# Performance work log

Measured on AMD Instinct MI355X. Metric: run time of the kernel, lower is better.

## Reference

```python
import jax, jax.numpy as jnp
import numpy as np

T_MIN, T_MAX = 0.6, 1.6
SIM_LO, SIM_HI = 0.5, 0.9
LN_EPS = 1e-5


def _layernorm(x, gamma, beta):
    mu = jnp.mean(x, axis=-1, keepdims=True)
    var = jnp.mean((x - mu) ** 2, axis=-1, keepdims=True)
    return (x - mu) * jax.lax.rsqrt(var + LN_EPS) * gamma + beta


def _cos_sim(a, b, eps=1e-8):
    num = jnp.sum(a * b, axis=-1)
    na = jnp.maximum(jnp.sqrt(jnp.sum(a * a, axis=-1)), eps)
    nb = jnp.maximum(jnp.sqrt(jnp.sum(b * b, axis=-1)), eps)
    return num / (na * nb)


def setup_inputs() -> dict:
    key = jax.random.key(0)
    B, L, D = 2, 4096, 512
    ks = jax.random.split(key, 10)
    s = 0.02
    return {
        "x": jax.random.normal(ks[0], (B, L, D), dtype=jnp.float32),
        "Wq": jax.random.normal(ks[1], (D, D), dtype=jnp.float32) * s,
        "Wk": jax.random.normal(ks[2], (D, D), dtype=jnp.float32) * s,
        "Wv": jax.random.normal(ks[3], (D, D), dtype=jnp.float32) * s,
        "Wp": jax.random.normal(ks[4], (D, D), dtype=jnp.float32) * s,
        "W1": jax.random.normal(ks[5], (4 * D, D), dtype=jnp.float32) * s,
        "b1": jnp.zeros((4 * D,), dtype=jnp.float32),
        "W2": jax.random.normal(ks[6], (D, 4 * D), dtype=jnp.float32) * s,
        "b2": jnp.zeros((D,), dtype=jnp.float32),
        "gamma": jnp.ones((D,), dtype=jnp.float32),
        "beta": jnp.zeros((D,), dtype=jnp.float32),
    }


def reference(x, Wq, Wk, Wv, Wp, W1, b1, W2, b2, gamma, beta):
    B, L, D = x.shape
    xn = _layernorm(x, gamma, beta)
    # TinyAttn with T=1.0, causal=True (torch Linear: x @ W.T)
    Q = jnp.einsum("bld,ed->ble", xn, Wq)
    K = jnp.einsum("bld,ed->ble", xn, Wk)
    V = jnp.einsum("bld,ed->ble", xn, Wv)
    scores = jnp.einsum("bld,bmd->blm", Q, K) / jnp.sqrt(jnp.asarray(D, x.dtype))
    causal = jnp.triu(jnp.ones((L, L), dtype=bool), 1)
    scores = jnp.where(causal, jnp.asarray(-1e30, x.dtype), scores)
    attn = jax.nn.softmax(scores, axis=-1)  # [B, L, L]
    out = jnp.einsum("blm,bmd->bld", attn, V)
    out = jnp.einsum("bld,ed->ble", out, Wp)
    ctx = x + out
    h = _layernorm(ctx, gamma, beta)
    h = jax.nn.gelu(jnp.einsum("bld,fd->blf", h, W1) + b1, approximate=False)
    ctx = ctx + jnp.einsum("blf,df->bld", h, W2) + b2

    # AdaptiveController on last-token attention row
    last_attn = attn[:, -1]  # [B, L]
    p = jnp.clip(last_attn, 1e-9, None)
    H = -jnp.sum(p * jnp.log(p), axis=-1)  # [B]
    Hn = (H - H.min()) / (H.max() - H.min() + 1e-9)
    Hm = jax.lax.stop_gradient(jnp.mean(Hn))  # detached in torch
    T = T_MIN + (T_MAX - T_MIN) * Hm
    sim_th = SIM_HI - (SIM_HI - SIM_LO) * Hm

    # UnconsciousStack: single forward -> stack holds only the just-pushed (K, V), detached.
    q_vec = jnp.mean(Q[:, -1], axis=0, keepdims=True)  # [1, D]
    K_rep = jax.lax.stop_gradient(jnp.mean(K, axis=1))  # [B, D]
    s = jnp.mean(_cos_sim(q_vec, K_rep))  # scalar
    hit = s >= sim_th

    K_cat = jnp.concatenate([K, jax.lax.stop_gradient(K)], axis=1)  # [B, 2L, D]
    V_cat = jnp.concatenate([V, jax.lax.stop_gradient(V)], axis=1)
    scores2 = jnp.einsum("bld,bmd->blm", Q, K_cat) / jnp.sqrt(jnp.asarray(D, x.dtype))
    attn2 = jax.nn.softmax(scores2 / T, axis=-1)  # [B, L, 2L], no causal mask
    reatt = jnp.einsum("blm,bmd->bld", attn2, V_cat)
    ctx = ctx + jnp.where(hit, reatt, jnp.zeros_like(reatt))
    return ctx
```

## Files before the change

kernel.cpp:

```cpp
#include <hip/hip_runtime.h>
#include <math.h>

#define BATCH 2
#define SEQ 4096
#define DIM 512
#define FF 2048
#define NROWS (BATCH*SEQ)
#define KT 32
#define RSQRT_D 0.044194173824159216f

typedef __attribute__((ext_vector_type(8))) short short8;
typedef __attribute__((ext_vector_type(4))) short short4v;
typedef __attribute__((ext_vector_type(4))) float f32x4;

__device__ __forceinline__ float gelu_f(float v) {
    return 0.5f * v * (1.0f + erff(v * 0.70710678118654752440f));
}
__device__ __forceinline__ short bf16b(float x) {
    union { float f; unsigned u; } c; c.f = x;
    unsigned r = (c.u + 0x7FFFu + ((c.u >> 16) & 1u)) >> 16;
    return (short)r;
}
__device__ __forceinline__ float bf16f(short h) {
    union { unsigned u; float f; } c; c.u = ((unsigned)(unsigned short)h) << 16;
    return c.f;
}
__device__ __forceinline__ void gload16(const void* g, void* l) {
    __builtin_amdgcn_global_load_lds(
        (const __attribute__((address_space(1))) unsigned int*)g,
        (__attribute__((address_space(3))) unsigned int*)l, 16, 0, 0);
}
__device__ __forceinline__ float blk_sum256(float v, volatile float* sm) {
    #pragma unroll
    for (int o = 32; o; o >>= 1) v += __shfl_xor(v, o);
    __syncthreads();
    if ((threadIdx.x & 63) == 0) sm[threadIdx.x >> 6] = v;
    __syncthreads();
    return sm[0] + sm[1] + sm[2] + sm[3];
}

__global__ __launch_bounds__(256) void f2bf_all(
        const float* __restrict__ Wq, const float* __restrict__ Wk,
        const float* __restrict__ Wv, const float* __restrict__ Wp,
        const float* __restrict__ W1, const float* __restrict__ W2,
        short* __restrict__ Wcat, short* __restrict__ Wpb,
        short* __restrict__ W1b, short* __restrict__ W2b)
{
    int i = blockIdx.x * 256 + threadIdx.x;
    const float* src; short* dst; int loc;
    if      (i <  32768) { src = Wq; dst = Wcat;          loc = i; }
    else if (i <  65536) { src = Wk; dst = Wcat + 262144; loc = i - 32768; }
    else if (i <  98304) { src = Wv; dst = Wcat + 524288; loc = i - 65536; }
    else if (i < 131072) { src = Wp; dst = Wpb;           loc = i - 98304; }
    else if (i < 262144) { src = W1; dst = W1b;           loc = i - 131072; }
    else                 { src = W2; dst = W2b;           loc = i - 262144; }
    const float4* p = (const float4*)(src + (size_t)loc * 8);
    float4 a = p[0], b = p[1];
    short8 r;
    r[0]=bf16b(a.x); r[1]=bf16b(a.y); r[2]=bf16b(a.z); r[3]=bf16b(a.w);
    r[4]=bf16b(b.x); r[5]=bf16b(b.y); r[6]=bf16b(b.z); r[7]=bf16b(b.w);
    *(short8*)(dst + (size_t)loc * 8) = r;
}

__global__ __launch_bounds__(256) void ln_kernel(const float* __restrict__ x,
        const float* __restrict__ g, const float* __restrict__ be,
        short* __restrict__ o)
{
    int row  = blockIdx.x * 4 + (threadIdx.x >> 6);
    int lane = threadIdx.x & 63;
    const float4* xr = (const float4*)(x + (size_t)row * DIM);
    float4 v0 = xr[lane*2], v1 = xr[lane*2+1];
    float s = v0.x+v0.y+v0.z+v0.w + v1.x+v1.y+v1.z+v1.w;
    #pragma unroll
    for (int off = 32; off; off >>= 1) s += __shfl_xor(s, off);
    float mu = s * (1.0f/DIM);
    float d[8] = {v0.x-mu, v0.y-mu, v0.z-mu, v0.w-mu, v1.x-mu, v1.y-mu, v1.z-mu, v1.w-mu};
    float q = 0.f;
    #pragma unroll
    for (int j = 0; j < 8; ++j) q += d[j]*d[j];
    #pragma unroll
    for (int off = 32; off; off >>= 1) q += __shfl_xor(q, off);
    float rs = rsqrtf(q * (1.0f/DIM) + 1e-5f);
    const float4* g4 = (const float4*)g;
    const float4* b4 = (const float4*)be;
    float4 ga = g4[lane*2], gb = g4[lane*2+1];
    float4 ba = b4[lane*2], bb = b4[lane*2+1];
    float gv[8] = {ga.x,ga.y,ga.z,ga.w, gb.x,gb.y,gb.z,gb.w};
    float bv[8] = {ba.x,ba.y,ba.z,ba.w, bb.x,bb.y,bb.z,bb.w};
    short8 r;
    #pragma unroll
    for (int j = 0; j < 8; ++j) r[j] = bf16b(d[j]*rs*gv[j] + bv[j]);
    *(short8*)(o + (size_t)row * DIM + lane*8) = r;
}

__global__ __launch_bounds__(256) void gemm_v2(
        const short* __restrict__ A, const short* __restrict__ W,
        const float* __restrict__ bias, const float* __restrict__ res,
        float* __restrict__ Cf, short* __restrict__ Cb,
        short* __restrict__ CbK, short* __restrict__ CbV,
        int K, int sa, int sw, int sc, int act, int accum)
{
    __shared__ short As[2][4096];
    __shared__ short Ws[2][4096];
    int tid = threadIdx.x;
    int m0 = blockIdx.y * 128, n0 = blockIdx.x * 128;
    int w = tid >> 6, lane = tid & 63;
    int wr = (w >> 1) * 64, wc = (w & 1) * 64;
    int lr = lane & 15, lg = lane >> 4;
    int srow = tid >> 2, skoff = (tid & 3) * 8;
    const short* Ab = A + (size_t)(m0 + srow) * sa + skoff;
    const short* Wb = W + (size_t)(n0 + srow) * sw + skoff;

    #define STAGE_G(buf, kk) do { \
        gload16(Ab + (kk),                    As[buf] + tid*8); \
        gload16(Ab + (size_t)64*sa + (kk),    As[buf] + 2048 + tid*8); \
        gload16(Wb + (kk),                    Ws[buf] + tid*8); \
        gload16(Wb + (size_t)64*sw + (kk),    Ws[buf] + 2048 + tid*8); } while(0)

    f32x4 acc[4][4];
    f32x4 zero = {0.f, 0.f, 0.f, 0.f};
    #pragma unroll
    for (int i = 0; i < 4; ++i)
        #pragma unroll
        for (int j = 0; j < 4; ++j) acc[i][j] = zero;

    STAGE_G(0, 0);
    __syncthreads();
    int cur = 0;
    for (int k0 = 0; k0 < K; k0 += 32) {
        if (k0 + 32 < K) STAGE_G(cur ^ 1, k0 + 32);
        short8 a[4], b[4];
        #pragma unroll
        for (int i = 0; i < 4; ++i) a[i] = *(const short8*)(As[cur] + (wr + i*16 + lr)*32 + lg*8);
        #pragma unroll
        for (int j = 0; j < 4; ++j) b[j] = *(const short8*)(Ws[cur] + (wc + j*16 + lr)*32 + lg*8);
        #pragma unroll
        for (int i = 0; i < 4; ++i)
            #pragma unroll
            for (int j = 0; j < 4; ++j)
                acc[i][j] = __builtin_amdgcn_mfma_f32_16x16x32_bf16(a[i], b[j], acc[i][j], 0, 0, 0);
        __syncthreads();
        cur ^= 1;
    }
    #undef STAGE_G

    #pragma unroll
    for (int i = 0; i < 4; ++i) {
        #pragma unroll
        for (int r = 0; r < 4; ++r) {
            size_t m = (size_t)m0 + wr + i*16 + lg*4 + r;
            #pragma unroll
            for (int j = 0; j < 4; ++j) {
                int n = n0 + wc + j*16 + lr;
                float v = acc[i][j][r];
                if (bias) v += bias[n];
                if (act)  v = gelu_f(v);
                if (CbK) {
                    int seg = n >> 9, nl = n & 511;
                    short* dst = (seg == 0) ? Cb : (seg == 1) ? CbK : CbV;
                    dst[m * 512 + nl] = bf16b(v);
                } else {
                    if (res) v += res[m * sc + n];
                    size_t idx = m * sc + n;
                    if (Cf) { if (accum) Cf[idx] += v; else Cf[idx] = v; }
                    if (Cb) Cb[idx] = bf16b(v);
                }
            }
        }
    }
}

__global__ __launch_bounds__(256) void vtrans(const short* __restrict__ V,
                                              short* __restrict__ Vt)
{
    __shared__ short t_s[64][72];
    int l0 = blockIdx.x * 64, d0 = blockIdx.y * 64, b = blockIdx.z;
    int t = threadIdx.x;
    const short* src = V + (size_t)b * SEQ * DIM;
    #pragma unroll
    for (int it = 0; it < 2; ++it) {
        int r = (t >> 3) + it * 32, c = (t & 7) * 8;
        *(short8*)&t_s[r][c] = *(const short8*)(src + (size_t)(l0 + r) * DIM + d0 + c);
    }
    __syncthreads();
    short* dst = Vt + (size_t)b * DIM * SEQ;
    #pragma unroll
    for (int it = 0; it < 2; ++it) {
        int r = (t >> 3) + it * 32, c = (t & 7) * 8;
        short8 v;
        #pragma unroll
        for (int j = 0; j < 8; ++j) v[j] = t_s[c + j][r];
        *(short8*)(dst + (size_t)(d0 + r) * SEQ + l0 + c) = v;
    }
}

__global__ __launch_bounds__(512, 2) void attn_v4(
        const short* __restrict__ Q, const short* __restrict__ K,
        const short* __restrict__ Vt, short* __restrict__ Opart,
        float* __restrict__ Mpart, float* __restrict__ Lpart,
        float scale, const float* __restrict__ scale_ptr,
        const float* __restrict__ gate, int causal, int NC, int ncs)
{
    if (gate && gate[0] == 0.0f) return;
    if (scale_ptr) scale = scale_ptr[0];
    extern __shared__ short lds[];
    short* k_s = lds;
    short* v_s = lds + 32768;
    short* p_s = lds + 65536;

    int tid = threadIdx.x, w = tid >> 6, lane = tid & 63;
    int rg = w >> 1, dh = w & 1;
    int lr = lane & 15, lg = lane >> 4;

    int bid = blockIdx.x;
    int c  = bid & (NC - 1);
    int b  = (bid >> ncs) & 1;
    int ip = bid >> (ncs + 1);
    int jj0 = ip, jj1 = 63 - ip;
    int TA = causal ? 2*(ip+1)  : 128;
    int TB = causal ? 2*(64-ip) : 128;
    int Ttot = TA + TB;
    int s0 = (Ttot * c) >> ncs, s1 = (Ttot * (c+1)) >> ncs;

    size_t bofs = (size_t)b * SEQ * DIM;
    size_t vofs = (size_t)b * DIM * SEQ;
    f32x4 zero = {0.f, 0.f, 0.f, 0.f};

    for (int sg = 0; sg < 2; ++sg) {
        int j  = sg ? jj1 : jj0;
        int ta = sg ? (max(s0, TA) - TA) : s0;
        int tb = sg ? (s1 - TA)          : min(s1, TA);
        if (ta >= tb) continue;
        int qw0 = j*64 + rg*16;

        short8 qf[16];
        #pragma unroll
        for (int kc = 0; kc < 16; ++kc)
            qf[kc] = *(const short8*)(Q + bofs + (size_t)(qw0 + lr)*DIM + kc*32 + lg*8);

        f32x4 o[16];
        #pragma unroll
        for (int df = 0; df < 16; ++df) o[df] = zero;
        float mreg[4] = {-1e30f,-1e30f,-1e30f,-1e30f};
        float lreg[4] = {0.f,0.f,0.f,0.f};
        int rowg[4];
        #pragma unroll
        for (int r = 0; r < 4; ++r) rowg[r] = qw0 + lg*4 + r;

        int cur = 0;
        {
            int k0s = ta * KT;
            #pragma unroll
            for (int s4 = 0; s4 < 4; ++s4) {
                int slot = tid + s4*512;
                int row = slot >> 6, cg = slot & 63;
                gload16(K + bofs + (size_t)(k0s + row)*DIM + ((cg ^ (row & 7)) << 3),
                        k_s + slot*8);
                int dpair = slot >> 3, low = slot & 7;
                int d = dpair*2 + (low & 1);
                int kg = (low >> 1) ^ (dpair & 3);
                gload16(Vt + vofs + (size_t)d*SEQ + k0s + kg*8,
                        v_s + slot*8);
            }
        }
        __syncthreads();

        for (int t = ta; t < tb; ++t) {
            int k0 = t * KT;
            if (t + 1 < tb) {
                int k0s = (t + 1) * KT;
                int bo = (cur ^ 1) * 16384;
                #pragma unroll
                for (int s4 = 0; s4 < 4; ++s4) {
                    int slot = tid + s4*512;
                    int row = slot >> 6, cg = slot & 63;
                    gload16(K + bofs + (size_t)(k0s + row)*DIM + ((cg ^ (row & 7)) << 3),
                            k_s + bo + slot*8);
                    int dpair = slot >> 3, low = slot & 7;
                    int d = dpair*2 + (low & 1);
                    int kg = (low >> 1) ^ (dpair & 3);
                    gload16(Vt + vofs + (size_t)d*SEQ + k0s + kg*8,
                            v_s + bo + slot*8);
                }
            }
            f32x4 ss[2];
            ss[0] = zero; ss[1] = zero;
            const short* kb = k_s + cur*16384;
            #pragma unroll
            for (int kc = 0; kc < 16; ++kc) {
                #pragma unroll
                for (int kf = 0; kf < 2; ++kf) {
                    int row = kf*16 + lr;
                    short8 kk = *(const short8*)(kb + row*512 + (((kc*4 + lg) ^ (row & 7)) << 3));
                    ss[kf] = __builtin_amdgcn_mfma_f32_16x16x32_bf16(qf[kc], kk, ss[kf], 0, 0, 0);
                }
            }
            bool needmask = causal && (k0 + KT - 1 > qw0);
            #pragma unroll
            for (int kf = 0; kf < 2; ++kf) {
                int key = k0 + kf*16 + lr;
                #pragma unroll
                for (int r = 0; r < 4; ++r) {
                    float sv = ss[kf][r] * scale;
                    if (needmask && key > rowg[r]) sv = -1e30f;
                    ss[kf][r] = sv;
                }
            }
            float pm[4];
            bool tg = false;
            #pragma unroll
            for (int r = 0; r < 4; ++r) {
                pm[r] = fmaxf(ss[0][r], ss[1][r]);
                tg |= (pm[r] > mreg[r] + 8.0f);
            }
            if (__any(tg)) {
                #pragma unroll
                for (int r = 0; r < 4; ++r) {
                    float v = pm[r];
                    v = fmaxf(v, __shfl_xor(v, 1));
                    v = fmaxf(v, __shfl_xor(v, 2));
                    v = fmaxf(v, __shfl_xor(v, 4));
                    v = fmaxf(v, __shfl_xor(v, 8));
                    float nm = fmaxf(mreg[r], v);
                    float fr = __expf(mreg[r] - nm);
                    mreg[r] = nm;
                    lreg[r] *= fr;
                    #pragma unroll
                    for (int df = 0; df < 16; ++df) o[df][r] *= fr;
                }
            }
            #pragma unroll
            for (int kf = 0; kf < 2; ++kf) {
                #pragma unroll
                for (int r = 0; r < 4; ++r) {
                    float sv = ss[kf][r];
                    float p = (sv < -1e29f) ? 0.0f : __expf(sv - mreg[r]);
                    lreg[r] += p;
                    int row = lg*4 + r;
                    int oct = kf*2 + (lr >> 3);
                    p_s[w*512 + row*32 + ((oct ^ (row & 3)) << 3) + (lr & 7)] = bf16b(p);
                }
            }
            short8 pa = *(const short8*)(p_s + w*512 + lr*32 + ((lg ^ (lr & 3)) << 3));
            const short* vb = v_s + cur*16384;
            #pragma unroll
            for (int df = 0; df < 16; ++df) {
                int d = dh*256 + df*16 + lr;
                int slot16 = (d >> 1)*8 + (((lg ^ ((d >> 1) & 3)) << 1) | (d & 1));
                short8 vv = *(const short8*)(vb + slot16*8);
                o[df] = __builtin_amdgcn_mfma_f32_16x16x32_bf16(pa, vv, o[df], 0, 0, 0);
            }
            __syncthreads();
            cur ^= 1;
        }

        #pragma unroll
        for (int r = 0; r < 4; ++r) {
            float v = lreg[r];
            v += __shfl_xor(v, 1);
            v += __shfl_xor(v, 2);
            v += __shfl_xor(v, 4);
            v += __shfl_xor(v, 8);
            lreg[r] = v;
        }
        int slot = (b*64 + j)*NC + c;
        size_t obase = ((size_t)slot*8 + w) * 4096;
        #pragma unroll
        for (int df = 0; df < 16; ++df) {
            short4v pk;
            #pragma unroll
            for (int r = 0; r < 4; ++r) pk[r] = bf16b(o[df][r]);
            *(short4v*)(Opart + obase + df*256 + lane*4) = pk;
        }
        if (dh == 0 && lr == 0) {
            #pragma unroll
            for (int r = 0; r < 4; ++r) {
                Mpart[slot*64 + rg*16 + lg*4 + r] = mreg[r];
                Lpart[slot*64 + rg*16 + lg*4 + r] = lreg[r];
            }
        }
    }
}

__global__ __launch_bounds__(256) void attn_merge(
        const short* __restrict__ Opart, const float* __restrict__ Mpart,
        const float* __restrict__ Lpart, short* __restrict__ attb,
        float* __restrict__ outf, const float* __restrict__ gate,
        int causal, int NC, int ncs)
{
    if (gate && gate[0] == 0.0f) return;
    __shared__ float wts[8][64];
    int j = blockIdx.x, dh = blockIdx.y, b = blockIdx.z;
    int tid = threadIdx.x;
    int ip = (j < 32) ? j : 63 - j;
    int TA = causal ? 2*(ip+1)  : 128;
    int TB = causal ? 2*(64-ip) : 128;
    int Ttot = TA + TB;
    int jstart = (j < 32) ? 0 : TA;
    int jend   = (j < 32) ? TA : Ttot;
    bool val[8];
    for (int c = 0; c < 8; ++c) {
        int sc = (Ttot * c) >> ncs, ec = (Ttot * (c+1)) >> ncs;
        val[c] = (c < NC) && (sc < jend) && (ec > jstart);
    }
    if (tid < 64) {
        float M = -1e30f;
        for (int c = 0; c < NC; ++c)
            if (val[c]) M = fmaxf(M, Mpart[((b*64 + j)*NC + c)*64 + tid]);
        float L = 0.f;
        for (int c = 0; c < NC; ++c)
            if (val[c]) L += Lpart[((b*64 + j)*NC + c)*64 + tid]
                           * __expf(Mpart[((b*64 + j)*NC + c)*64 + tid] - M);
        float invL = 1.0f / L;
        for (int c = 0; c < NC; ++c)
            wts[c][tid] = val[c]
                ? __expf(Mpart[((b*64 + j)*NC + c)*64 + tid] - M) * invL : 0.0f;
    }
    __syncthreads();
    int wv = tid >> 6, lane = tid & 63, lg = lane >> 4, lr = lane & 15;
    int region = wv*2 + dh;
    for (int df = 0; df < 16; ++df) {
        float acc[4] = {0.f, 0.f, 0.f, 0.f};
        for (int c = 0; c < NC; ++c) {
            if (!val[c]) continue;
            size_t idx = ((size_t)((b*64 + j)*NC + c)*8 + region)*4096 + df*256 + lane*4;
            short4v v = *(const short4v*)(Opart + idx);
            #pragma unroll
            for (int r = 0; r < 4; ++r)
                acc[r] += wts[c][wv*16 + lg*4 + r] * bf16f(v[r]);
        }
        #pragma unroll
        for (int r = 0; r < 4; ++r) {
            int row = j*64 + wv*16 + lg*4 + r;
            int d = dh*256 + df*16 + lr;
            size_t oidx = (size_t)b*SEQ*DIM + (size_t)row*DIM + d;
            if (attb) attb[oidx] = bf16b(acc[r]);
            else      outf[oidx] += acc[r];
        }
    }
}

__global__ __launch_bounds__(256) void lastrow_scores(const short* __restrict__ Q,
        const short* __restrict__ K, float* __restrict__ slast)
{
    __shared__ float q_l[DIM];
    int b = blockIdx.y;
    int m = blockIdx.x * 256 + threadIdx.x;
    for (int i = threadIdx.x; i < DIM; i += 256)
        q_l[i] = bf16f(Q[((size_t)b*SEQ + SEQ-1)*DIM + i]);
    __syncthreads();
    const short* kr = K + ((size_t)b*SEQ + m) * DIM;
    float s = 0.f;
    for (int d = 0; d < DIM; d += 8) {
        short8 k8 = *(const short8*)(kr + d);
        #pragma unroll
        for (int j = 0; j < 8; ++j) s += q_l[d + j] * bf16f(k8[j]);
    }
    slast[(size_t)b*SEQ + m] = s * RSQRT_D;
}

__global__ __launch_bounds__(256) void entropy_kernel(const float* __restrict__ slast,
        float* __restrict__ H)
{
    __shared__ float sm[4];
    int b = blockIdx.x, t = threadIdx.x;
    const float* s = slast + (size_t)b * SEQ;
    float v[16];
    float mx = -1e30f;
    #pragma unroll
    for (int j = 0; j < 16; ++j) { v[j] = s[t + j*256]; mx = fmaxf(mx, v[j]); }
    #pragma unroll
    for (int o = 32; o; o >>= 1) mx = fmaxf(mx, __shfl_xor(mx, o));
    __syncthreads();
    if ((t & 63) == 0) sm[t >> 6] = mx;
    __syncthreads();
    mx = fmaxf(fmaxf(sm[0], sm[1]), fmaxf(sm[2], sm[3]));
    float se = 0.f;
    #pragma unroll
    for (int j = 0; j < 16; ++j) { v[j] = expf(v[j] - mx); se += v[j]; }
    se = blk_sum256(se, sm);
    float inv = 1.0f / se;
    float h = 0.f;
    #pragma unroll
    for (int j = 0; j < 16; ++j) {
        float p = fmaxf(v[j] * inv, 1e-9f);
        h -= p * logf(p);
    }
    h = blk_sum256(h, sm);
    if (t == 0) H[b] = h;
}

__global__ __launch_bounds__(256) void krep_partial(const short* __restrict__ K,
        float* __restrict__ part)
{
    int b = blockIdx.y, j = blockIdx.x, t = threadIdx.x;
    size_t base = ((size_t)b*SEQ + (size_t)j*64) * DIM;
    float s0 = 0.f, s1 = 0.f;
    for (int r = 0; r < 64; ++r) {
        s0 += bf16f(K[base + (size_t)r*DIM + t]);
        s1 += bf16f(K[base + (size_t)r*DIM + t + 256]);
    }
    size_t o = (size_t)(b*64 + j) * DIM;
    part[o + t] = s0; part[o + t + 256] = s1;
}

__global__ __launch_bounds__(256) void scalar_kernel(const short* __restrict__ Qb,
        const float* __restrict__ part, const float* __restrict__ Hent,
        float* __restrict__ gsc)
{
    __shared__ float sm[4];
    __shared__ float sims[BATCH];
    int t = threadIdx.x;
    float qv0 = 0.5f*(bf16f(Qb[((size_t)0*SEQ + SEQ-1)*DIM + t])     + bf16f(Qb[((size_t)1*SEQ + SEQ-1)*DIM + t]));
    float qv1 = 0.5f*(bf16f(Qb[((size_t)0*SEQ + SEQ-1)*DIM + t+256]) + bf16f(Qb[((size_t)1*SEQ + SEQ-1)*DIM + t+256]));
    for (int b = 0; b < BATCH; ++b) {
        float k0 = 0.f, k1 = 0.f;
        for (int j = 0; j < 64; ++j) {
            k0 += part[(size_t)(b*64+j)*DIM + t];
            k1 += part[(size_t)(b*64+j)*DIM + t + 256];
        }
        k0 *= (1.0f/SEQ); k1 *= (1.0f/SEQ);
        float num = blk_sum256(qv0*k0 + qv1*k1, sm);
        float qq  = blk_sum256(qv0*qv0 + qv1*qv1, sm);
        float kk  = blk_sum256(k0*k0 + k1*k1, sm);
        if (t == 0) {
            float na = fmaxf(sqrtf(qq), 1e-8f);
            float nb = fmaxf(sqrtf(kk), 1e-8f);
            sims[b] = num / (na * nb);
        }
        __syncthreads();
    }
    if (t == 0) {
        float H0 = Hent[0], H1 = Hent[1];
        float mn = fminf(H0, H1), mx = fmaxf(H0, H1);
        float den = (mx - mn) + 1e-9f;
        float Hm = 0.5f*((H0 - mn)/den + (H1 - mn)/den);
        float T  = 0.6f + (1.6f - 0.6f) * Hm;
        float th = 0.9f - (0.9f - 0.5f) * Hm;
        float s  = 0.5f * (sims[0] + sims[1]);
        gsc[0] = (s >= th) ? 1.0f : 0.0f;
        gsc[1] = 1.0f / (sqrtf((float)DIM) * T);
    }
}

extern "C" void kernel_launch(void* const* d_in, const int* in_sizes, int n_in,
                              void* d_out, int out_size, void* d_ws, size_t ws_size,
                              hipStream_t stream)
{
    (void)in_sizes; (void)n_in; (void)out_size;
    const float* x     = (const float*)d_in[0];
    const float* Wq    = (const float*)d_in[1];
    const float* Wk    = (const float*)d_in[2];
    const float* Wv    = (const float*)d_in[3];
    const float* Wp    = (const float*)d_in[4];
    const float* W1    = (const float*)d_in[5];
    const float* b1    = (const float*)d_in[6];
    const float* W2    = (const float*)d_in[7];
    const float* b2    = (const float*)d_in[8];
    const float* gamma = (const float*)d_in[9];
    const float* beta  = (const float*)d_in[10];
    float* out = (float*)d_out;

    const size_t NT = (size_t)NROWS * DIM;
    short* bws   = (short*)d_ws;
    short* Qbf   = bws;
    short* Kbf   = Qbf + NT;
    short* Vt    = Kbf + NT;
    short* att   = Vt + NT;
    short* Wcat  = att + NT;
    short* Wpb   = Wcat + 786432;
    short* W1b   = Wpb + 262144;
    short* W2b   = W1b + 1048576;
    float* slast = (float*)(W2b + 1048576);
    float* Hent  = slast + 8192;
    float* kpart = Hent + 8;
    float* gsc   = kpart + 65536;

    float* Mpart8 = gsc + 8;
    size_t ml8 = (size_t)128 * 8 * 64;
    short* xn8 = (short*)(Mpart8 + 2*ml8);
    size_t opart8_end = ((size_t)(xn8 - bws)) + (size_t)1024 * 8 * 4096;
    int NC = (ws_size >= opart8_end * 2 + 1024) ? 8 : 4;
    int ncs = (NC == 8) ? 3 : 2;
    size_t mlsz = (size_t)128 * NC * 64;
    float* Mpart = gsc + 8;
    float* Lpart = Mpart + mlsz;
    short* xn_bf = (short*)(Lpart + mlsz);
    short* h1    = xn_bf + NT;
    short* Opart = xn_bf;

    size_t ffn_full_end = ((size_t)(h1 - bws) + (size_t)NROWS * FF) * 2;
    int ffn_full = (ws_size >= ffn_full_end + 1024);

    const int ATTN_LDS = 139264;
    hipFuncSetAttribute((const void*)attn_v4,
                        hipFuncAttributeMaxDynamicSharedMemorySize, ATTN_LDS);

    f2bf_all<<<1536, 256, 0, stream>>>(Wq, Wk, Wv, Wp, W1, W2, Wcat, Wpb, W1b, W2b);

    ln_kernel<<<NROWS/4, 256, 0, stream>>>(x, gamma, beta, xn_bf);

    gemm_v2<<<dim3(1536/128, NROWS/128), 256, 0, stream>>>(
        xn_bf, Wcat, nullptr, nullptr, nullptr, Qbf, Kbf, att,
        DIM, DIM, DIM, DIM, 0, 0);
    vtrans<<<dim3(SEQ/64, DIM/64, BATCH), 256, 0, stream>>>(att, Vt);

    attn_v4<<<64*NC, 512, ATTN_LDS, stream>>>(Qbf, Kbf, Vt, Opart, Mpart, Lpart,
                                              RSQRT_D, nullptr, nullptr, 1, NC, ncs);
    attn_merge<<<dim3(64, 2, BATCH), 256, 0, stream>>>(Opart, Mpart, Lpart, att, nullptr,
                                                       nullptr, 1, NC, ncs);

    lastrow_scores<<<dim3(SEQ/256, BATCH), 256, 0, stream>>>(Qbf, Kbf, slast);
    entropy_kernel<<<BATCH, 256, 0, stream>>>(slast, Hent);

    gemm_v2<<<dim3(DIM/128, NROWS/128), 256, 0, stream>>>(
        att, Wpb, nullptr, x, out, nullptr, nullptr, nullptr,
        DIM, DIM, DIM, DIM, 0, 0);

    ln_kernel<<<NROWS/4, 256, 0, stream>>>(out, gamma, beta, xn_bf);

    if (ffn_full) {
        gemm_v2<<<dim3(FF/128, NROWS/128), 256, 0, stream>>>(
            xn_bf, W1b, b1, nullptr, nullptr, h1, nullptr, nullptr,
            DIM, DIM, DIM, FF, 1, 0);
        gemm_v2<<<dim3(DIM/128, NROWS/128), 256, 0, stream>>>(
            h1, W2b, b2, nullptr, out, nullptr, nullptr, nullptr,
            FF, FF, FF, DIM, 0, 1);
    } else {
        for (int c = 0; c < 2; ++c) {
            gemm_v2<<<dim3(1024/128, NROWS/128), 256, 0, stream>>>(
                xn_bf, W1b + (size_t)c*1024*DIM, b1 + c*1024, nullptr,
                nullptr, h1, nullptr, nullptr,
                DIM, DIM, DIM, 1024, 1, 0);
            gemm_v2<<<dim3(DIM/128, NROWS/128), 256, 0, stream>>>(
                h1, W2b + (size_t)c*1024, (c == 0) ? b2 : nullptr, nullptr,
                out, nullptr, nullptr, nullptr,
                1024, 1024, FF, DIM, 0, 1);
        }
    }

    krep_partial<<<dim3(64, BATCH), 256, 0, stream>>>(Kbf, kpart);
    scalar_kernel<<<1, 256, 0, stream>>>(Qbf, kpart, Hent, gsc);

    attn_v4<<<64*NC, 512, ATTN_LDS, stream>>>(Qbf, Kbf, Vt, Opart, Mpart, Lpart,
                                              0.0f, gsc + 1, gsc, 0, NC, ncs);
    attn_merge<<<dim3(64, 2, BATCH), 256, 0, stream>>>(Opart, Mpart, Lpart, nullptr, out,
                                                       gsc, 0, NC, ncs);
}
```

Baseline: 404.3 us.

## Single-buffer K/V in attention with staggered prefetch to halve LDS

Replaces the double-buffered K and V LDS tiles with single buffers. The next K tile is loaded right after QK^T finishes and the next V tile right after PV finishes, so each load overlaps the other half of the iteration. LDS per block drops from 139264 to 73728 bytes, which is meant to let two 512-thread blocks fit per CU as the launch bounds request. It also changes the P-tile swizzle to reduce LDS bank conflicts. The cost is an extra barrier per iteration and less latency hiding for each tile's load.

Result: no change. 404.3 us (+0.0%).

```diff
diff --git a/kernel.cpp b/kernel.cpp
--- a/kernel.cpp
+++ b/kernel.cpp
@@ -194,7 +194,7 @@
     }
 }
 
-__global__ __launch_bounds__(512, 2) void attn_v4(
+__global__ __launch_bounds__(512, 2) void attn_v7(
         const short* __restrict__ Q, const short* __restrict__ K,
         const short* __restrict__ Vt, short* __restrict__ Opart,
         float* __restrict__ Mpart, float* __restrict__ Lpart,
@@ -205,8 +205,8 @@
     if (scale_ptr) scale = scale_ptr[0];
     extern __shared__ short lds[];
     short* k_s = lds;
-    short* v_s = lds + 32768;
-    short* p_s = lds + 65536;
+    short* v_s = lds + 16384;
+    short* p_s = lds + 32768;
 
     int tid = threadIdx.x, w = tid >> 6, lane = tid & 63;
     int rg = w >> 1, dh = w & 1;
@@ -247,7 +247,6 @@
         #pragma unroll
         for (int r = 0; r < 4; ++r) rowg[r] = qw0 + lg*4 + r;
 
-        int cur = 0;
         {
             int k0s = ta * KT;
             #pragma unroll
@@ -267,32 +266,27 @@
 
         for (int t = ta; t < tb; ++t) {
             int k0 = t * KT;
-            if (t + 1 < tb) {
+            bool pre = (t + 1 < tb);
+            f32x4 ss[2];
+            ss[0] = zero; ss[1] = zero;
+            #pragma unroll
+            for (int kc = 0; kc < 16; ++kc) {
+                #pragma unroll
+                for (int kf = 0; kf < 2; ++kf) {
+                    int row = kf*16 + lr;
+                    short8 kk = *(const short8*)(k_s + row*512 + (((kc*4 + lg) ^ (row & 7)) << 3));
+                    ss[kf] = __builtin_amdgcn_mfma_f32_16x16x32_bf16(qf[kc], kk, ss[kf], 0, 0, 0);
+                }
+            }
+            __syncthreads();
+            if (pre) {
                 int k0s = (t + 1) * KT;
-                int bo = (cur ^ 1) * 16384;
                 #pragma unroll
                 for (int s4 = 0; s4 < 4; ++s4) {
                     int slot = tid + s4*512;
                     int row = slot >> 6, cg = slot & 63;
                     gload16(K + bofs + (size_t)(k0s + row)*DIM + ((cg ^ (row & 7)) << 3),
-                            k_s + bo + slot*8);
-                    int dpair = slot >> 3, low = slot & 7;
-                    int d = dpair*2 + (low & 1);
-                    int kg = (low >> 1) ^ (dpair & 3);
-                    gload16(Vt + vofs + (size_t)d*SEQ + k0s + kg*8,
-                            v_s + bo + slot*8);
-                }
-            }
-            f32x4 ss[2];
-            ss[0] = zero; ss[1] = zero;
-            const short* kb = k_s + cur*16384;
-            #pragma unroll
-            for (int kc = 0; kc < 16; ++kc) {
-                #pragma unroll
-                for (int kf = 0; kf < 2; ++kf) {
-                    int row = kf*16 + lr;
-                    short8 kk = *(const short8*)(kb + row*512 + (((kc*4 + lg) ^ (row & 7)) << 3));
-                    ss[kf] = __builtin_amdgcn_mfma_f32_16x16x32_bf16(qf[kc], kk, ss[kf], 0, 0, 0);
+                            k_s + slot*8);
                 }
             }
             bool needmask = causal && (k0 + KT - 1 > qw0);
@@ -338,20 +332,31 @@
                     lreg[r] += p;
                     int row = lg*4 + r;
                     int oct = kf*2 + (lr >> 3);
-                    p_s[w*512 + row*32 + ((oct ^ (row & 3)) << 3) + (lr & 7)] = bf16b(p);
+                    p_s[w*512 + row*32 + ((oct ^ r ^ (lg & 3)) << 3) + (lr & 7)] = bf16b(p);
                 }
             }
-            short8 pa = *(const short8*)(p_s + w*512 + lr*32 + ((lg ^ (lr & 3)) << 3));
-            const short* vb = v_s + cur*16384;
+            short8 pa = *(const short8*)(p_s + w*512 + lr*32
+                         + ((lg ^ (lr & 3) ^ ((lr >> 2) & 3)) << 3));
             #pragma unroll
             for (int df = 0; df < 16; ++df) {
                 int d = dh*256 + df*16 + lr;
                 int slot16 = (d >> 1)*8 + (((lg ^ ((d >> 1) & 3)) << 1) | (d & 1));
-                short8 vv = *(const short8*)(vb + slot16*8);
+                short8 vv = *(const short8*)(v_s + slot16*8);
                 o[df] = __builtin_amdgcn_mfma_f32_16x16x32_bf16(pa, vv, o[df], 0, 0, 0);
             }
             __syncthreads();
-            cur ^= 1;
+            if (pre) {
+                int k0s = (t + 1) * KT;
+                #pragma unroll
+                for (int s4 = 0; s4 < 4; ++s4) {
+                    int slot = tid + s4*512;
+                    int dpair = slot >> 3, low = slot & 7;
+                    int d = dpair*2 + (low & 1);
+                    int kg = (low >> 1) ^ (dpair & 3);
+                    gload16(Vt + vofs + (size_t)d*SEQ + k0s + kg*8,
+                            v_s + slot*8);
+                }
+            }
         }
 
         #pragma unroll
@@ -592,8 +597,8 @@
     size_t ffn_full_end = ((size_t)(h1 - bws) + (size_t)NROWS * FF) * 2;
     int ffn_full = (ws_size >= ffn_full_end + 1024);
 
-    const int ATTN_LDS = 139264;
-    hipFuncSetAttribute((const void*)attn_v4,
+    const int ATTN_LDS = 73728;
+    hipFuncSetAttribute((const void*)attn_v7,
                         hipFuncAttributeMaxDynamicSharedMemorySize, ATTN_LDS);
 
     f2bf_all<<<1536, 256, 0, stream>>>(Wq, Wk, Wv, Wp, W1, W2, Wcat, Wpb, W1b, W2b);
@@ -605,7 +610,7 @@
         DIM, DIM, DIM, DIM, 0, 0);
     vtrans<<<dim3(SEQ/64, DIM/64, BATCH), 256, 0, stream>>>(att, Vt);
 
-    attn_v4<<<64*NC, 512, ATTN_LDS, stream>>>(Qbf, Kbf, Vt, Opart, Mpart, Lpart,
+    attn_v7<<<64*NC, 512, ATTN_LDS, stream>>>(Qbf, Kbf, Vt, Opart, Mpart, Lpart,
                                               RSQRT_D, nullptr, nullptr, 1, NC, ncs);
     attn_merge<<<dim3(64, 2, BATCH), 256, 0, stream>>>(Opart, Mpart, Lpart, att, nullptr,
                                                        nullptr, 1, NC, ncs);
@@ -642,7 +647,7 @@
     krep_partial<<<dim3(64, BATCH), 256, 0, stream>>>(Kbf, kpart);
     scalar_kernel<<<1, 256, 0, stream>>>(Qbf, kpart, Hent, gsc);
 
-    attn_v4<<<64*NC, 512, ATTN_LDS, stream>>>(Qbf, Kbf, Vt, Opart, Mpart, Lpart,
+    attn_v7<<<64*NC, 512, ATTN_LDS, stream>>>(Qbf, Kbf, Vt, Opart, Mpart, Lpart,
                                               0.0f, gsc + 1, gsc, 0, NC, ncs);
     attn_merge<<<dim3(64, 2, BATCH), 256, 0, stream>>>(Opart, Mpart, Lpart, nullptr, out,
                                                        gsc, 0, NC, ncs);
```

## Split QK^T head dimension across wave pairs and exchange partial scores via LDS

Applied to the files above, without the earlier changes.

In the attention kernel, the two waves sharing a row group previously each computed the full 512-wide QK^T for the same rows. Now each wave computes half of the head dimension and they exchange partial scores through a new LDS region with a barrier, halving redundant score MFMAs and Q register footprint. The P-tile swizzle in LDS is also changed to reduce bank conflicts. The cost is an extra LDS round trip, a barrier per key tile, and more dynamic LDS, which may limit occupancy.

New measurement: 406.4 us. About the same (+0.5%).

```diff
diff --git a/kernel.cpp b/kernel.cpp
--- a/kernel.cpp
+++ b/kernel.cpp
@@ -93,6 +93,7 @@
     *(short8*)(o + (size_t)row * DIM + lane*8) = r;
 }
 
+template<int TAG>
 __global__ __launch_bounds__(256) void gemm_v2(
         const short* __restrict__ A, const short* __restrict__ W,
         const float* __restrict__ bias, const float* __restrict__ res,
@@ -194,7 +195,7 @@
     }
 }
 
-__global__ __launch_bounds__(512, 2) void attn_v4(
+__global__ __launch_bounds__(512, 2) void attn_v8(
         const short* __restrict__ Q, const short* __restrict__ K,
         const short* __restrict__ Vt, short* __restrict__ Opart,
         float* __restrict__ Mpart, float* __restrict__ Lpart,
@@ -204,9 +205,10 @@
     if (gate && gate[0] == 0.0f) return;
     if (scale_ptr) scale = scale_ptr[0];
     extern __shared__ short lds[];
-    short* k_s = lds;
-    short* v_s = lds + 32768;
-    short* p_s = lds + 65536;
+    short* k_s  = lds;
+    short* v_s  = lds + 32768;
+    short* p_s  = lds + 65536;
+    float* ss_s = (float*)(lds + 69632);
 
     int tid = threadIdx.x, w = tid >> 6, lane = tid & 63;
     int rg = w >> 1, dh = w & 1;
@@ -233,10 +235,11 @@
         if (ta >= tb) continue;
         int qw0 = j*64 + rg*16;
 
-        short8 qf[16];
-        #pragma unroll
-        for (int kc = 0; kc < 16; ++kc)
-            qf[kc] = *(const short8*)(Q + bofs + (size_t)(qw0 + lr)*DIM + kc*32 + lg*8);
+        short8 qf[8];
+        #pragma unroll
+        for (int kc = 0; kc < 8; ++kc)
+            qf[kc] = *(const short8*)(Q + bofs + (size_t)(qw0 + lr)*DIM
+                                      + dh*256 + kc*32 + lg*8);
 
         f32x4 o[16];
         #pragma unroll
@@ -287,24 +290,32 @@
             ss[0] = zero; ss[1] = zero;
             const short* kb = k_s + cur*16384;
             #pragma unroll
-            for (int kc = 0; kc < 16; ++kc) {
+            for (int kc = 0; kc < 8; ++kc) {
                 #pragma unroll
                 for (int kf = 0; kf < 2; ++kf) {
                     int row = kf*16 + lr;
-                    short8 kk = *(const short8*)(kb + row*512 + (((kc*4 + lg) ^ (row & 7)) << 3));
+                    int dg = dh*32 + kc*4 + lg;
+                    short8 kk = *(const short8*)(kb + row*512 + ((dg ^ (row & 7)) << 3));
                     ss[kf] = __builtin_amdgcn_mfma_f32_16x16x32_bf16(qf[kc], kk, ss[kf], 0, 0, 0);
                 }
             }
+            *(f32x4*)(ss_s + w*512 + lane*8)     = ss[0];
+            *(f32x4*)(ss_s + w*512 + lane*8 + 4) = ss[1];
+            asm volatile("s_waitcnt lgkmcnt(0)" ::: "memory");
+            __builtin_amdgcn_s_barrier();
+            __builtin_amdgcn_sched_barrier(0);
+            f32x4 po0 = *(const f32x4*)(ss_s + (w^1)*512 + lane*8);
+            f32x4 po1 = *(const f32x4*)(ss_s + (w^1)*512 + lane*8 + 4);
             bool needmask = causal && (k0 + KT - 1 > qw0);
             #pragma unroll
-            for (int kf = 0; kf < 2; ++kf) {
-                int key = k0 + kf*16 + lr;
-                #pragma unroll
-                for (int r = 0; r < 4; ++r) {
-                    float sv = ss[kf][r] * scale;
-                    if (needmask && key > rowg[r]) sv = -1e30f;
-                    ss[kf][r] = sv;
+            for (int r = 0; r < 4; ++r) {
+                float s0v = (ss[0][r] + po0[r]) * scale;
+                float s1v = (ss[1][r] + po1[r]) * scale;
+                if (needmask) {
+                    if (k0 + lr      > rowg[r]) s0v = -1e30f;
+                    if (k0 + 16 + lr > rowg[r]) s1v = -1e30f;
                 }
+                ss[0][r] = s0v; ss[1][r] = s1v;
             }
             float pm[4];
             bool tg = false;
@@ -338,10 +349,11 @@
                     lreg[r] += p;
                     int row = lg*4 + r;
                     int oct = kf*2 + (lr >> 3);
-                    p_s[w*512 + row*32 + ((oct ^ (row & 3)) << 3) + (lr & 7)] = bf16b(p);
+                    p_s[w*512 + row*32 + ((oct ^ r ^ (lg & 3)) << 3) + (lr & 7)] = bf16b(p);
                 }
             }
-            short8 pa = *(const short8*)(p_s + w*512 + lr*32 + ((lg ^ (lr & 3)) << 3));
+            short8 pa = *(const short8*)(p_s + w*512 + lr*32
+                         + ((lg ^ (lr & 3) ^ ((lr >> 2) & 3)) << 3));
             const short* vb = v_s + cur*16384;
             #pragma unroll
             for (int df = 0; df < 16; ++df) {
@@ -592,20 +604,20 @@
     size_t ffn_full_end = ((size_t)(h1 - bws) + (size_t)NROWS * FF) * 2;
     int ffn_full = (ws_size >= ffn_full_end + 1024);
 
-    const int ATTN_LDS = 139264;
-    hipFuncSetAttribute((const void*)attn_v4,
+    const int ATTN_LDS = 155648;
+    hipFuncSetAttribute((const void*)attn_v8,
                         hipFuncAttributeMaxDynamicSharedMemorySize, ATTN_LDS);
 
     f2bf_all<<<1536, 256, 0, stream>>>(Wq, Wk, Wv, Wp, W1, W2, Wcat, Wpb, W1b, W2b);
 
     ln_kernel<<<NROWS/4, 256, 0, stream>>>(x, gamma, beta, xn_bf);
 
-    gemm_v2<<<dim3(1536/128, NROWS/128), 256, 0, stream>>>(
+    gemm_v2<0><<<dim3(1536/128, NROWS/128), 256, 0, stream>>>(
         xn_bf, Wcat, nullptr, nullptr, nullptr, Qbf, Kbf, att,
         DIM, DIM, DIM, DIM, 0, 0);
     vtrans<<<dim3(SEQ/64, DIM/64, BATCH), 256, 0, stream>>>(att, Vt);
 
-    attn_v4<<<64*NC, 512, ATTN_LDS, stream>>>(Qbf, Kbf, Vt, Opart, Mpart, Lpart,
+    attn_v8<<<64*NC, 512, ATTN_LDS, stream>>>(Qbf, Kbf, Vt, Opart, Mpart, Lpart,
                                               RSQRT_D, nullptr, nullptr, 1, NC, ncs);
     attn_merge<<<dim3(64, 2, BATCH), 256, 0, stream>>>(Opart, Mpart, Lpart, att, nullptr,
                                                        nullptr, 1, NC, ncs);
@@ -613,26 +625,26 @@
     lastrow_scores<<<dim3(SEQ/256, BATCH), 256, 0, stream>>>(Qbf, Kbf, slast);
     entropy_kernel<<<BATCH, 256, 0, stream>>>(slast, Hent);
 
-    gemm_v2<<<dim3(DIM/128, NROWS/128), 256, 0, stream>>>(
+    gemm_v2<1><<<dim3(DIM/128, NROWS/128), 256, 0, stream>>>(
         att, Wpb, nullptr, x, out, nullptr, nullptr, nullptr,
         DIM, DIM, DIM, DIM, 0, 0);
 
     ln_kernel<<<NROWS/4, 256, 0, stream>>>(out, gamma, beta, xn_bf);
 
     if (ffn_full) {
-        gemm_v2<<<dim3(FF/128, NROWS/128), 256, 0, stream>>>(
+        gemm_v2<2><<<dim3(FF/128, NROWS/128), 256, 0, stream>>>(
             xn_bf, W1b, b1, nullptr, nullptr, h1, nullptr, nullptr,
             DIM, DIM, DIM, FF, 1, 0);
-        gemm_v2<<<dim3(DIM/128, NROWS/128), 256, 0, stream>>>(
+        gemm_v2<3><<<dim3(DIM/128, NROWS/128), 256, 0, stream>>>(
             h1, W2b, b2, nullptr, out, nullptr, nullptr, nullptr,
             FF, FF, FF, DIM, 0, 1);
     } else {
         for (int c = 0; c < 2; ++c) {
-            gemm_v2<<<dim3(1024/128, NROWS/128), 256, 0, stream>>>(
+            gemm_v2<2><<<dim3(1024/128, NROWS/128), 256, 0, stream>>>(
                 xn_bf, W1b + (size_t)c*1024*DIM, b1 + c*1024, nullptr,
                 nullptr, h1, nullptr, nullptr,
                 DIM, DIM, DIM, 1024, 1, 0);
-            gemm_v2<<<dim3(DIM/128, NROWS/128), 256, 0, stream>>>(
+            gemm_v2<3><<<dim3(DIM/128, NROWS/128), 256, 0, stream>>>(
                 h1, W2b + (size_t)c*1024, (c == 0) ? b2 : nullptr, nullptr,
                 out, nullptr, nullptr, nullptr,
                 1024, 1024, FF, DIM, 0, 1);
@@ -642,7 +654,7 @@
     krep_partial<<<dim3(64, BATCH), 256, 0, stream>>>(Kbf, kpart);
     scalar_kernel<<<1, 256, 0, stream>>>(Qbf, kpart, Hent, gsc);
 
-    attn_v4<<<64*NC, 512, ATTN_LDS, stream>>>(Qbf, Kbf, Vt, Opart, Mpart, Lpart,
+    attn_v8<<<64*NC, 512, ATTN_LDS, stream>>>(Qbf, Kbf, Vt, Opart, Mpart, Lpart,
                                               0.0f, gsc + 1, gsc, 0, NC, ncs);
     attn_merge<<<dim3(64, 2, BATCH), 256, 0, stream>>>(Opart, Mpart, Lpart, nullptr, out,
                                                        gsc, 0, NC, ncs);
```
